# Optimization experiments

Hardware: AMD Instinct MI355X
Metric: run time of the kernel (lower is better)

The kernel has to match this reference:

```python
import jax, jax.numpy as jnp
import numpy as np

BATCH = 65536
SEQ_LEN = 32
EMB = 64
H = 128


def setup_inputs() -> dict:
    key = jax.random.key(0)
    ks = jax.random.split(key, 12)
    s = 0.05
    inp = {
        "last_pos": jax.random.normal(ks[0], (BATCH, 2), jnp.float32),
        "last_pos_rel": jax.random.normal(ks[1], (BATCH, 2), jnp.float32),
        "hh": jax.random.normal(ks[2], (1, BATCH, H), jnp.float32),
        "ch": jax.random.normal(ks[3], (1, BATCH, H), jnp.float32),
        "seq_start_end": jnp.sort(jax.random.randint(ks[4], (256, 2), 0, BATCH), axis=0),
        # LSTM(embedding_dim -> h_dim), PyTorch gate order [i, f, g, o]
        "w_ih": jax.random.normal(ks[5], (4 * H, EMB), jnp.float32) * s,
        "w_hh": jax.random.normal(ks[6], (4 * H, H), jnp.float32) * s,
        "b_ih": jax.random.normal(ks[7], (4 * H,), jnp.float32) * s,
        "b_hh": jax.random.normal(ks[8], (4 * H,), jnp.float32) * s,
        # spatial_embedding: Linear(2 -> EMB)
        "w_emb": jax.random.normal(ks[9], (EMB, 2), jnp.float32) * s,
        "b_emb": jax.random.normal(ks[10], (EMB,), jnp.float32) * s,
        # hidden2pos: Linear(H -> 2)
        "w_pos": jax.random.normal(ks[11], (2, H), jnp.float32) * s,
        "b_pos": jnp.zeros((2,), jnp.float32),
    }
    return inp


def _decode(last_pos, last_pos_rel, hh, ch, w_ih, w_hh, b_ih, b_hh,
            w_emb, b_emb, w_pos, b_pos):
    h0, c0 = hh[0], ch[0]                      # (B, H)
    x0 = last_pos_rel @ w_emb.T + b_emb        # (B, EMB)
    b = b_ih + b_hh

    def step(carry, _):
        h, c, lp, x = carry
        gates = x @ w_ih.T + h @ w_hh.T + b    # (B, 4H)
        i, f, g, o = jnp.split(gates, 4, axis=-1)
        c2 = jax.nn.sigmoid(f) * c + jax.nn.sigmoid(i) * jnp.tanh(g)
        h2 = jax.nn.sigmoid(o) * jnp.tanh(c2)
        rel = h2 @ w_pos.T + b_pos             # (B, 2)
        cur = rel + lp
        x2 = rel @ w_emb.T + b_emb             # next decoder input embedding
        return (h2, c2, cur, x2), rel

    (hN, cN, _, _), rels = jax.lax.scan(step, (h0, c0, last_pos, x0),
                                        None, length=SEQ_LEN)
    # rels: (SEQ_LEN, B, 2) == pred_traj_fake_rel; hN[None]: (1, B, H)
    return rels, hN[None]


def reference(last_pos, last_pos_rel, hh, ch, seq_start_end,
              w_ih, w_hh, b_ih, b_hh, w_emb, b_emb, w_pos, b_pos):
    # seq_start_end is unused when pool_every_timestep=False
    return _decode(last_pos, last_pos_rel, hh, ch,
                   w_ih, w_hh, b_ih, b_hh, w_emb, b_emb, w_pos, b_pos)
```

## Files before the change

### kernel.cpp

```cpp
#include <hip/hip_runtime.h>

#define B_TOT 65536
#define SEQ   32

typedef __bf16 bf16_8 __attribute__((ext_vector_type(8)));
typedef __bf16 bf16_4 __attribute__((ext_vector_type(4)));
typedef float  float4v __attribute__((ext_vector_type(4)));
typedef float  float2v __attribute__((ext_vector_type(2)));

#define SC1 (-1.4426950408889634f)
#define SC2 (-2.8853900817779268f)

__device__ inline unsigned short f2bf(float f){
    unsigned u = __builtin_bit_cast(unsigned, f);
    u += 0x7FFFu + ((u >> 16) & 1u);
    return (unsigned short)(u >> 16);
}

__global__ void prep_kernel(const float* __restrict__ w_ih,
                            const float* __restrict__ w_hh,
                            const float* __restrict__ b_ih,
                            const float* __restrict__ b_hh,
                            const float* __restrict__ w_emb,
                            const float* __restrict__ b_emb,
                            const float* __restrict__ w_pos,
                            const float* __restrict__ b_pos,
                            unsigned short* __restrict__ weff,
                            float* __restrict__ beff,
                            float* __restrict__ m2,
                            unsigned short* __restrict__ wposA)
{
    int n = threadIdx.x;
    float m20 = 0.f, m21 = 0.f, bi = 0.f;
    for (int e = 0; e < 64; ++e){
        float wv = w_ih[n*64 + e];
        m20 += w_emb[e*2 + 0] * wv;
        m21 += w_emb[e*2 + 1] * wv;
        bi  += b_emb[e] * wv;
    }
    float sc = ((n >> 7) == 2) ? SC2 : SC1;
    m2[n]       = m20 * sc;
    m2[512 + n] = m21 * sc;
    beff[n] = (b_ih[n] + b_hh[n] + bi + b_pos[0]*m20 + b_pos[1]*m21) * sc;
    for (int k = 0; k < 128; ++k){
        float wv = w_hh[n*128 + k] + w_pos[k]*m20 + w_pos[128 + k]*m21;
        weff[n*128 + k] = f2bf(wv * sc);
    }
    if (n < 256) wposA[n] = f2bf(w_pos[n]);
    for (int idx = n; idx < 14*128; idx += 512) wposA[256 + idx] = 0;
}

__global__ __launch_bounds__(256, 2) void dec_kernel(
    const float* __restrict__ lpr,
    const float* __restrict__ hh,
    const float* __restrict__ ch,
    const float* __restrict__ b_pos,
    const unsigned short* __restrict__ wposA,
    const unsigned short* __restrict__ weff,
    const float* __restrict__ beff,
    const float* __restrict__ m2,
    float* __restrict__ out)
{
    __shared__ __align__(16) unsigned short lh[2][16][136];
    __shared__ float ubuf[16][2];
    __shared__ __align__(16) float hsh[16][128];

    const int tid  = threadIdx.x;
    const int w    = tid >> 6;
    const int lane = tid & 63;
    const int q    = lane >> 4;
    const int l    = lane & 15;
    const int row0 = blockIdx.x << 4;
    const int batch = row0 + l;

    bf16_8 wA[8][4];
    float4v bias4[8];
#pragma unroll
    for (int t8 = 0; t8 < 8; ++t8){
        int nbase = ((t8 >> 1) << 7) + 32*w + ((t8 & 1) << 4);
        int gA = nbase + l;
#pragma unroll
        for (int kt = 0; kt < 4; ++kt)
            wA[t8][kt] = *(const bf16_8*)(weff + (gA << 7) + kt*32 + (q << 3));
        bias4[t8] = *(const float4v*)(beff + nbase + (q << 2));
    }

    bf16_8 wpA[4];
#pragma unroll
    for (int kt = 0; kt < 4; ++kt)
        wpA[kt] = *(const bf16_8*)(wposA + (l << 7) + kt*32 + (q << 3));
    const float bp0 = b_pos[0], bp1 = b_pos[1];

    float4v cst[2];
#pragma unroll
    for (int X = 0; X < 2; ++X)
        cst[X] = *(const float4v*)(ch + (batch << 7) + 32*w + 16*X + (q << 2));

    bf16_8 b[4];
#pragma unroll
    for (int kt = 0; kt < 4; ++kt){
        const float* ph = hh + (batch << 7) + kt*32 + (q << 3);
        float4v h0 = *(const float4v*)ph;
        float4v h1 = *(const float4v*)(ph + 4);
        bf16_8 t;
        t[0]=(__bf16)h0[0]; t[1]=(__bf16)h0[1]; t[2]=(__bf16)h0[2]; t[3]=(__bf16)h0[3];
        t[4]=(__bf16)h1[0]; t[5]=(__bf16)h1[1]; t[6]=(__bf16)h1[2]; t[7]=(__bf16)h1[3];
        b[kt] = t;
    }

    if (w == 0){
        float4v r = {0.f, 0.f, 0.f, 0.f};
#pragma unroll
        for (int kt = 0; kt < 4; ++kt)
            r = __builtin_amdgcn_mfma_f32_16x16x32_bf16(wpA[kt], b[kt], r, 0, 0, 0);
        if (q == 0){
            float2v lp = *(const float2v*)(lpr + (batch << 1));
            ubuf[l][0] = lp[0] - (r[0] + bp0);
            ubuf[l][1] = lp[1] - (r[1] + bp1);
        }
    }
    __syncthreads();

    float4v acc[8];

    auto do_gates = [&](){
#pragma unroll
        for (int t8 = 0; t8 < 8; ++t8)
            acc[t8] = __builtin_amdgcn_mfma_f32_16x16x32_bf16(wA[t8][0], b[0], bias4[t8], 0, 0, 0);
#pragma unroll
        for (int kt = 1; kt < 4; ++kt)
#pragma unroll
            for (int t8 = 0; t8 < 8; ++t8)
                acc[t8] = __builtin_amdgcn_mfma_f32_16x16x32_bf16(wA[t8][kt], b[kt], acc[t8], 0, 0, 0);
    };

    auto do_elem_write = [&](int buf, bool finalh){
#pragma unroll
        for (int X = 0; X < 2; ++X){
            bf16_4 hv;
#pragma unroll
            for (int r4 = 0; r4 < 4; ++r4){
                float ei = __builtin_amdgcn_exp2f(acc[0 + X][r4]);
                float ef = __builtin_amdgcn_exp2f(acc[2 + X][r4]);
                float eg = __builtin_amdgcn_exp2f(acc[4 + X][r4]);
                float pi_ = 1.f + ei, pf = 1.f + ef;
                float pg  = 1.f + eg, mg = 1.f - eg;
                float t2  = pi_ * pg;
                float den = pf * t2;
                float num = fmaf(cst[X][r4], t2, pf * mg);
                float c2  = num * __builtin_amdgcn_rcpf(den);
                float eo  = __builtin_amdgcn_exp2f(acc[6 + X][r4]);
                float ec  = __builtin_amdgcn_exp2f(c2 * SC2);
                float po = 1.f + eo, pc = 1.f + ec, mc = 1.f - ec;
                float h2 = mc * __builtin_amdgcn_rcpf(po * pc);
                cst[X][r4] = c2;
                hv[r4] = (__bf16)h2;
                if (finalh) hsh[l][32*w + 16*X + (q << 2) + r4] = h2;
            }
            *(bf16_4*)&lh[buf][l][32*w + 16*X + (q << 2)] = hv;
        }
    };

    auto reload_and_rel = [&](int buf, int t){
#pragma unroll
        for (int kt = 0; kt < 4; ++kt)
            b[kt] = *(const bf16_8*)&lh[buf][l][kt*32 + (q << 3)];
        if (w == (t & 3)){
            float4v r = {0.f, 0.f, 0.f, 0.f};
#pragma unroll
            for (int kt = 0; kt < 4; ++kt)
                r = __builtin_amdgcn_mfma_f32_16x16x32_bf16(wpA[kt], b[kt], r, 0, 0, 0);
            if (q == 0){
                float2v rv;
                rv[0] = r[0] + bp0;
                rv[1] = r[1] + bp1;
                *(float2v*)(out + t*(B_TOT*2) + (batch << 1)) = rv;
            }
        }
    };

    do_gates();
    {
        float u0 = ubuf[l][0], u1 = ubuf[l][1];
#pragma unroll
        for (int t8 = 0; t8 < 8; ++t8){
            int g0 = ((t8 >> 1) << 7) + 32*w + ((t8 & 1) << 4) + (q << 2);
            float4v ma = *(const float4v*)(m2 + g0);
            float4v mb = *(const float4v*)(m2 + 512 + g0);
#pragma unroll
            for (int r4 = 0; r4 < 4; ++r4)
                acc[t8][r4] += u0*ma[r4] + u1*mb[r4];
        }
    }
    do_elem_write(1, false);
    __syncthreads();
    reload_and_rel(1, 0);

    for (int t = 1; t < SEQ; ++t){
        do_gates();
        do_elem_write((t + 1) & 1, t == SEQ - 1);
        __syncthreads();
        reload_and_rel((t + 1) & 1, t);
    }

    __syncthreads();
    {
        int r = tid >> 4, c8 = (tid & 15) << 3;
        float4v v0 = *(const float4v*)&hsh[r][c8];
        float4v v1 = *(const float4v*)&hsh[r][c8 + 4];
        float* po = out + SEQ*B_TOT*2 + ((row0 + r) << 7) + c8;
        *(float4v*)po = v0;
        *(float4v*)(po + 4) = v1;
    }
}

extern "C" void kernel_launch(void* const* d_in, const int* in_sizes, int n_in,
                              void* d_out, int out_size, void* d_ws, size_t ws_size,
                              hipStream_t stream)
{
    (void)in_sizes; (void)n_in; (void)out_size; (void)ws_size;

    const float* lpr   = (const float*)d_in[1];
    const float* hh    = (const float*)d_in[2];
    const float* ch    = (const float*)d_in[3];
    const float* w_ih  = (const float*)d_in[5];
    const float* w_hh  = (const float*)d_in[6];
    const float* b_ih  = (const float*)d_in[7];
    const float* b_hh  = (const float*)d_in[8];
    const float* w_emb = (const float*)d_in[9];
    const float* b_emb = (const float*)d_in[10];
    const float* w_pos = (const float*)d_in[11];
    const float* b_pos = (const float*)d_in[12];

    unsigned short* weff  = (unsigned short*)d_ws;
    float* beff           = (float*)((char*)d_ws + 131072);
    float* m2             = (float*)((char*)d_ws + 131072 + 2048);
    unsigned short* wposA = (unsigned short*)((char*)d_ws + 131072 + 2048 + 4096);

    hipLaunchKernelGGL(prep_kernel, dim3(1), dim3(512), 0, stream,
                       w_ih, w_hh, b_ih, b_hh, w_emb, b_emb, w_pos, b_pos,
                       weff, beff, m2, wposA);
    hipLaunchKernelGGL(dec_kernel, dim3(B_TOT/16), dim3(256), 0, stream,
                       lpr, hh, ch, b_pos, wposA, weff, beff, m2,
                       (float*)d_out);
}
```

Before: 497.3 us.

## Split gate work across 8 waves per block and swizzle hidden-state LDS layout

Result: slower. 960.8 us (+93.2%).

```diff
diff --git a/kernel.cpp b/kernel.cpp
--- a/kernel.cpp
+++ b/kernel.cpp
@@ -50,7 +50,7 @@
     for (int idx = n; idx < 14*128; idx += 512) wposA[256 + idx] = 0;
 }
 
-__global__ __launch_bounds__(256, 2) void dec_kernel(
+__global__ __launch_bounds__(512, 4) void dec_kernel(
     const float* __restrict__ lpr,
     const float* __restrict__ hh,
     const float* __restrict__ ch,
@@ -61,9 +61,11 @@
     const float* __restrict__ m2,
     float* __restrict__ out)
 {
-    __shared__ __align__(16) unsigned short lh[2][16][136];
+    __shared__ __align__(16) unsigned short lh[2][16][128];
     __shared__ float ubuf[16][2];
-    __shared__ __align__(16) float hsh[16][128];
+    __shared__ __align__(16) float hsh[16][132];
+    __shared__ float biasS[512];
+    __shared__ __align__(16) unsigned short wposS[16*128];
 
     const int tid  = threadIdx.x;
     const int w    = tid >> 6;
@@ -72,29 +74,21 @@
     const int l    = lane & 15;
     const int row0 = blockIdx.x << 4;
     const int batch = row0 + l;
-
-    bf16_8 wA[8][4];
-    float4v bias4[8];
-#pragma unroll
-    for (int t8 = 0; t8 < 8; ++t8){
-        int nbase = ((t8 >> 1) << 7) + 32*w + ((t8 & 1) << 4);
-        int gA = nbase + l;
+    const int hb   = w << 4;
+
+    biasS[tid] = beff[tid];
+    *(uint2*)&wposS[tid << 2] = *(const uint2*)(wposA + (tid << 2));
+
+    bf16_8 wA[4][4];
+#pragma unroll
+    for (int g = 0; g < 4; ++g){
+        int gr = (g << 7) + hb + l;
 #pragma unroll
         for (int kt = 0; kt < 4; ++kt)
-            wA[t8][kt] = *(const bf16_8*)(weff + (gA << 7) + kt*32 + (q << 3));
-        bias4[t8] = *(const float4v*)(beff + nbase + (q << 2));
-    }
-
-    bf16_8 wpA[4];
-#pragma unroll
-    for (int kt = 0; kt < 4; ++kt)
-        wpA[kt] = *(const bf16_8*)(wposA + (l << 7) + kt*32 + (q << 3));
-    const float bp0 = b_pos[0], bp1 = b_pos[1];
-
-    float4v cst[2];
-#pragma unroll
-    for (int X = 0; X < 2; ++X)
-        cst[X] = *(const float4v*)(ch + (batch << 7) + 32*w + 16*X + (q << 2));
+            wA[g][kt] = *(const bf16_8*)(weff + (gr << 7) + kt*32 + (q << 3));
+    }
+
+    float4v cst = *(const float4v*)(ch + (batch << 7) + hb + (q << 2));
 
     bf16_8 b[4];
 #pragma unroll
@@ -107,12 +101,19 @@
         t[4]=(__bf16)h1[0]; t[5]=(__bf16)h1[1]; t[6]=(__bf16)h1[2]; t[7]=(__bf16)h1[3];
         b[kt] = t;
     }
+    const float bp0 = b_pos[0], bp1 = b_pos[1];
+
+    __syncthreads();
 
     if (w == 0){
+        bf16_8 wp[4];
+#pragma unroll
+        for (int kt = 0; kt < 4; ++kt)
+            wp[kt] = *(const bf16_8*)&wposS[(l << 7) + kt*32 + (q << 3)];
         float4v r = {0.f, 0.f, 0.f, 0.f};
 #pragma unroll
         for (int kt = 0; kt < 4; ++kt)
-            r = __builtin_amdgcn_mfma_f32_16x16x32_bf16(wpA[kt], b[kt], r, 0, 0, 0);
+            r = __builtin_amdgcn_mfma_f32_16x16x32_bf16(wp[kt], b[kt], r, 0, 0, 0);
         if (q == 0){
             float2v lp = *(const float2v*)(lpr + (batch << 1));
             ubuf[l][0] = lp[0] - (r[0] + bp0);
@@ -121,55 +122,62 @@
     }
     __syncthreads();
 
-    float4v acc[8];
+    float4v acc[4];
 
     auto do_gates = [&](){
 #pragma unroll
-        for (int t8 = 0; t8 < 8; ++t8)
-            acc[t8] = __builtin_amdgcn_mfma_f32_16x16x32_bf16(wA[t8][0], b[0], bias4[t8], 0, 0, 0);
+        for (int g = 0; g < 4; ++g){
+            volatile const float* bp = &biasS[(g << 7) + hb + (q << 2)];
+            float4v c0 = {bp[0], bp[1], bp[2], bp[3]};
+            acc[g] = __builtin_amdgcn_mfma_f32_16x16x32_bf16(wA[g][0], b[0], c0, 0, 0, 0);
+        }
 #pragma unroll
         for (int kt = 1; kt < 4; ++kt)
 #pragma unroll
-            for (int t8 = 0; t8 < 8; ++t8)
-                acc[t8] = __builtin_amdgcn_mfma_f32_16x16x32_bf16(wA[t8][kt], b[kt], acc[t8], 0, 0, 0);
+            for (int g = 0; g < 4; ++g)
+                acc[g] = __builtin_amdgcn_mfma_f32_16x16x32_bf16(wA[g][kt], b[kt], acc[g], 0, 0, 0);
     };
 
     auto do_elem_write = [&](int buf, bool finalh){
-#pragma unroll
-        for (int X = 0; X < 2; ++X){
-            bf16_4 hv;
-#pragma unroll
-            for (int r4 = 0; r4 < 4; ++r4){
-                float ei = __builtin_amdgcn_exp2f(acc[0 + X][r4]);
-                float ef = __builtin_amdgcn_exp2f(acc[2 + X][r4]);
-                float eg = __builtin_amdgcn_exp2f(acc[4 + X][r4]);
-                float pi_ = 1.f + ei, pf = 1.f + ef;
-                float pg  = 1.f + eg, mg = 1.f - eg;
-                float t2  = pi_ * pg;
-                float den = pf * t2;
-                float num = fmaf(cst[X][r4], t2, pf * mg);
-                float c2  = num * __builtin_amdgcn_rcpf(den);
-                float eo  = __builtin_amdgcn_exp2f(acc[6 + X][r4]);
-                float ec  = __builtin_amdgcn_exp2f(c2 * SC2);
-                float po = 1.f + eo, pc = 1.f + ec, mc = 1.f - ec;
-                float h2 = mc * __builtin_amdgcn_rcpf(po * pc);
-                cst[X][r4] = c2;
-                hv[r4] = (__bf16)h2;
-                if (finalh) hsh[l][32*w + 16*X + (q << 2) + r4] = h2;
-            }
-            *(bf16_4*)&lh[buf][l][32*w + 16*X + (q << 2)] = hv;
-        }
+        bf16_4 hv;
+#pragma unroll
+        for (int r4 = 0; r4 < 4; ++r4){
+            float ei = __builtin_amdgcn_exp2f(acc[0][r4]);
+            float ef = __builtin_amdgcn_exp2f(acc[1][r4]);
+            float eg = __builtin_amdgcn_exp2f(acc[2][r4]);
+            float pi_ = 1.f + ei, pf = 1.f + ef;
+            float pg  = 1.f + eg, mg = 1.f - eg;
+            float t2  = pi_ * pg;
+            float den = pf * t2;
+            float num = fmaf(cst[r4], t2, pf * mg);
+            float c2  = num * __builtin_amdgcn_rcpf(den);
+            float eo  = __builtin_amdgcn_exp2f(acc[3][r4]);
+            float ec  = __builtin_amdgcn_exp2f(c2 * SC2);
+            float po = 1.f + eo, pc = 1.f + ec, mc = 1.f - ec;
+            float h2 = mc * __builtin_amdgcn_rcpf(po * pc);
+            cst[r4] = c2;
+            hv[r4] = (__bf16)h2;
+            if (finalh) hsh[l][hb + (q << 2) + r4] = h2;
+        }
+        int pcol = ((((w << 1) | (q >> 1)) ^ l) << 3) | ((q & 1) << 2);
+        *(bf16_4*)&lh[buf][l][pcol] = hv;
     };
 
     auto reload_and_rel = [&](int buf, int t){
 #pragma unroll
-        for (int kt = 0; kt < 4; ++kt)
-            b[kt] = *(const bf16_8*)&lh[buf][l][kt*32 + (q << 3)];
-        if (w == (t & 3)){
+        for (int kt = 0; kt < 4; ++kt){
+            int pcol = (((kt << 2) | q) ^ l) << 3;
+            b[kt] = *(const bf16_8*)&lh[buf][l][pcol];
+        }
+        if (w == (t & 7)){
+            bf16_8 wp[4];
+#pragma unroll
+            for (int kt = 0; kt < 4; ++kt)
+                wp[kt] = *(const bf16_8*)&wposS[(l << 7) + kt*32 + (q << 3)];
             float4v r = {0.f, 0.f, 0.f, 0.f};
 #pragma unroll
             for (int kt = 0; kt < 4; ++kt)
-                r = __builtin_amdgcn_mfma_f32_16x16x32_bf16(wpA[kt], b[kt], r, 0, 0, 0);
+                r = __builtin_amdgcn_mfma_f32_16x16x32_bf16(wp[kt], b[kt], r, 0, 0, 0);
             if (q == 0){
                 float2v rv;
                 rv[0] = r[0] + bp0;
@@ -183,13 +191,13 @@
     {
         float u0 = ubuf[l][0], u1 = ubuf[l][1];
 #pragma unroll
-        for (int t8 = 0; t8 < 8; ++t8){
-            int g0 = ((t8 >> 1) << 7) + 32*w + ((t8 & 1) << 4) + (q << 2);
+        for (int g = 0; g < 4; ++g){
+            int g0 = (g << 7) + hb + (q << 2);
             float4v ma = *(const float4v*)(m2 + g0);
             float4v mb = *(const float4v*)(m2 + 512 + g0);
 #pragma unroll
             for (int r4 = 0; r4 < 4; ++r4)
-                acc[t8][r4] += u0*ma[r4] + u1*mb[r4];
+                acc[g][r4] += u0*ma[r4] + u1*mb[r4];
         }
     }
     do_elem_write(1, false);
@@ -205,12 +213,9 @@
 
     __syncthreads();
     {
-        int r = tid >> 4, c8 = (tid & 15) << 3;
-        float4v v0 = *(const float4v*)&hsh[r][c8];
-        float4v v1 = *(const float4v*)&hsh[r][c8 + 4];
-        float* po = out + SEQ*B_TOT*2 + ((row0 + r) << 7) + c8;
-        *(float4v*)po = v0;
-        *(float4v*)(po + 4) = v1;
+        int r = tid >> 5, c4 = (tid & 31) << 2;
+        float4v v = *(const float4v*)&hsh[r][c4];
+        *(float4v*)(out + SEQ*B_TOT*2 + ((row0 + r) << 7) + c4) = v;
     }
 }
 
@@ -240,7 +245,7 @@
     hipLaunchKernelGGL(prep_kernel, dim3(1), dim3(512), 0, stream,
                        w_ih, w_hh, b_ih, b_hh, w_emb, b_emb, w_pos, b_pos,
                        weff, beff, m2, wposA);
-    hipLaunchKernelGGL(dec_kernel, dim3(B_TOT/16), dim3(256), 0, stream,
+    hipLaunchKernelGGL(dec_kernel, dim3(B_TOT/16), dim3(512), 0, stream,
                        lpr, hh, ch, b_pos, wposA, weff, beff, m2,
                        (float*)d_out);
 }
```
